# Optimization experiments

Hardware: AMD Instinct MI355X
Metric: run time of the kernel (lower is better)

The kernel has to match this reference:

```python
import jax, jax.numpy as jnp
import numpy as np

D = 1024      # in_dim
HS = 64       # head_size
H = 16        # num_heads
B, S = 2, 2048


def setup_inputs() -> dict:
    key = jax.random.key(0)
    k1, k2, k3, k4, k5, k6 = jax.random.split(key, 6)
    scale = 1.0 / np.sqrt(D)
    x = jax.random.normal(k1, (B, S, D), dtype=jnp.float32)
    # Stacked per-head projection weights (torch Linear weight is [out,in];
    # random init so layout only needs to be consistent). query weight exists
    # in the torch module but is never used (source bug), so it is omitted.
    Wk = jax.random.normal(k2, (H, D, HS), dtype=jnp.float32) * scale
    Wv = jax.random.normal(k3, (H, D, HS), dtype=jnp.float32) * scale
    Wproj = jax.random.normal(k4, (H * HS, D), dtype=jnp.float32) * (1.0 / np.sqrt(H * HS))
    bproj = jax.random.normal(k5, (D,), dtype=jnp.float32) * 0.01
    return {"x": x, "Wk": Wk, "Wv": Wv, "Wproj": Wproj, "bproj": bproj}


def reference(x, Wk, Wv, Wproj, bproj):
    # Faithful to source: k = key(x); q = value(x); v = value(x)  (q == v, no softmax)
    k = jnp.einsum("bsd,hde->bhse", x, Wk)   # [B,H,S,HS]
    v = jnp.einsum("bsd,hde->bhse", x, Wv)   # [B,H,S,HS]
    q = v
    inv_sqrt = jnp.asarray(HS, x.dtype) ** -0.5
    wei = jnp.einsum("bhse,bhte->bhst", q, k) * inv_sqrt  # [B,H,S,S], unnormalized
    out = jnp.einsum("bhst,bhte->bhse", wei, v)            # [B,H,S,HS]
    # concat heads: [B,S,H*HS]
    out = jnp.transpose(out, (0, 2, 1, 3)).reshape(x.shape[0], x.shape[1], H * HS)
    return out @ Wproj + bproj  # [B,S,D]
```

## Files before the change

### kernel.cpp

```cpp
#include <hip/hip_runtime.h>

#define B_ 2
#define S_ 2048
#define D_ 1024
#define H_ 16
#define HS_ 64
#define HD_ 1024
#define SPLIT 8
#define BS_ (B_*S_)

typedef __attribute__((ext_vector_type(8))) short short8_t;
typedef __attribute__((ext_vector_type(4))) float float4_t;

__device__ inline unsigned short f32_to_bf16(float f) {
  unsigned int u = __float_as_uint(f);
  u += 0x7FFF + ((u >> 16) & 1);
  return (unsigned short)(u >> 16);
}
__device__ inline float bf16_to_f32(unsigned short s) {
  return __uint_as_float(((unsigned int)s) << 16);
}

__device__ inline void async_copy16(const void* g, void* lds) {
  __builtin_amdgcn_global_load_lds(
      (const __attribute__((address_space(1))) void*)g,
      (__attribute__((address_space(3))) void*)lds, 16, 0, 0);
}

__global__ __launch_bounds__(256) void convert_x_kernel(
    const float* __restrict__ x, unsigned short* __restrict__ xb) {
  int idx = blockIdx.x * 256 + threadIdx.x;
  float4 v = ((const float4*)x)[idx];
  ushort4 o;
  o.x = f32_to_bf16(v.x); o.y = f32_to_bf16(v.y);
  o.z = f32_to_bf16(v.z); o.w = f32_to_bf16(v.w);
  ((ushort4*)xb)[idx] = o;
}

__global__ __launch_bounds__(256) void wkvt_kernel(
    const float* __restrict__ Wk, const float* __restrict__ Wv,
    unsigned short* __restrict__ Wkvt) {
  const int h = blockIdx.x >> 4;
  const int d0 = (blockIdx.x & 15) * 64;
  const int tid = threadIdx.x;
  __shared__ float lds[64][65];
#pragma unroll
  for (int i = 0; i < 16; ++i) {
    int idx = tid + i * 256; int dd = idx >> 6, e = idx & 63;
    lds[e][dd] = Wk[((size_t)h * D_ + d0 + dd) * HS_ + e];
  }
  __syncthreads();
#pragma unroll
  for (int i = 0; i < 16; ++i) {
    int idx = tid + i * 256; int e = idx >> 6, dd = idx & 63;
    Wkvt[((size_t)h * 128 + e) * D_ + d0 + dd] = f32_to_bf16(lds[e][dd]);
  }
  __syncthreads();
#pragma unroll
  for (int i = 0; i < 16; ++i) {
    int idx = tid + i * 256; int dd = idx >> 6, e = idx & 63;
    lds[e][dd] = Wv[((size_t)h * D_ + d0 + dd) * HS_ + e];
  }
  __syncthreads();
#pragma unroll
  for (int i = 0; i < 16; ++i) {
    int idx = tid + i * 256; int e = idx >> 6, dd = idx & 63;
    Wkvt[((size_t)h * 128 + 64 + e) * D_ + d0 + dd] = f32_to_bf16(lds[e][dd]);
  }
}

__global__ __launch_bounds__(256) void kv_mfma_kernel(
    const unsigned short* __restrict__ xb,
    const unsigned short* __restrict__ Wkvt,
    unsigned short* __restrict__ Kb,
    unsigned short* __restrict__ Vb) {
  const int blk = blockIdx.x;
  const int stile = blk & 31;
  const int h = blk >> 5;
  const int s0 = stile * 128;
  const int tid = threadIdx.x;
  const int lane = tid & 63;
  const int wid = tid >> 6;
  const int wm = wid & 1, wn = wid >> 1;
  const int quad = lane >> 4, l16 = lane & 15;
  const int arow = lane >> 2;
  const int acol = (lane & 3) * 8;

  __shared__ __align__(16) unsigned short As[128 * 32];
  __shared__ __align__(16) unsigned short Bs[128 * 32];

  float4_t acc[4][4];
  const float4_t fz = {0.f, 0.f, 0.f, 0.f};
#pragma unroll
  for (int i = 0; i < 4; ++i)
#pragma unroll
    for (int j = 0; j < 4; ++j) acc[i][j] = fz;

  for (int k0 = 0; k0 < D_; k0 += 32) {
#pragma unroll
    for (int i = 0; i < 2; ++i) {
      int r = wid * 32 + i * 16 + arow;
      async_copy16(xb + (size_t)(s0 + r) * D_ + k0 + acol,
                   As + (wid * 32 + i * 16) * 32);
      async_copy16(Wkvt + ((size_t)h * 128 + r) * D_ + k0 + acol,
                   Bs + (wid * 32 + i * 16) * 32);
    }
    __syncthreads();
    short8_t a[4], b[4];
#pragma unroll
    for (int mi = 0; mi < 4; ++mi)
      a[mi] = *(const short8_t*)(As + (wm * 64 + mi * 16 + l16) * 32 + quad * 8);
#pragma unroll
    for (int ni = 0; ni < 4; ++ni)
      b[ni] = *(const short8_t*)(Bs + (wn * 64 + ni * 16 + l16) * 32 + quad * 8);
#pragma unroll
    for (int mi = 0; mi < 4; ++mi)
#pragma unroll
      for (int ni = 0; ni < 4; ++ni)
        acc[mi][ni] = __builtin_amdgcn_mfma_f32_16x16x32_bf16(
            a[mi], b[ni], acc[mi][ni], 0, 0, 0);
    __syncthreads();
  }
  unsigned short* dst = (wn == 0) ? Kb : Vb;
#pragma unroll
  for (int mi = 0; mi < 4; ++mi)
#pragma unroll
    for (int ni = 0; ni < 4; ++ni) {
      int c = h * 64 + ni * 16 + l16;
      int rowb = s0 + wm * 64 + mi * 16 + quad * 4;
#pragma unroll
      for (int r = 0; r < 4; ++r)
        dst[(size_t)(rowb + r) * HD_ + c] = f32_to_bf16(acc[mi][ni][r]);
    }
}

__global__ __launch_bounds__(256) void m_partial_kernel(
    const unsigned short* __restrict__ Kb, const unsigned short* __restrict__ Vb,
    float* __restrict__ Mpart) {
  const int blk = blockIdx.x;
  const int h = blk & 15;
  const int b = (blk >> 4) & 1;
  const int split = blk >> 5;
  const int tid = threadIdx.x;
  const int tx = tid & 15, ty = tid >> 4;
  __shared__ float Ks[64][68];
  __shared__ float Vs[64][68];
  float acc[4][4] = {};
  const int sBase = split * (S_ / SPLIT);
  for (int sc = 0; sc < S_ / SPLIT; sc += 64) {
#pragma unroll
    for (int i = 0; i < 16; ++i) {
      int idx = tid + i * 256;
      int r = idx >> 6, c = idx & 63;
      size_t g = (size_t)(b * S_ + sBase + sc + r) * HD_ + h * HS_ + c;
      Ks[r][c] = bf16_to_f32(Kb[g]);
      Vs[r][c] = bf16_to_f32(Vb[g]);
    }
    __syncthreads();
#pragma unroll
    for (int ss = 0; ss < 64; ++ss) {
      const float4 a4 = *(const float4*)&Ks[ss][ty * 4];
      const float4 b4 = *(const float4*)&Vs[ss][tx * 4];
      const float a[4] = {a4.x, a4.y, a4.z, a4.w};
      const float bb[4] = {b4.x, b4.y, b4.z, b4.w};
#pragma unroll
      for (int i = 0; i < 4; ++i)
#pragma unroll
        for (int j = 0; j < 4; ++j) acc[i][j] += a[i] * bb[j];
    }
    __syncthreads();
  }
  float* dst = Mpart + ((size_t)(split * B_ + b) * H_ + h) * HS_ * HS_;
#pragma unroll
  for (int i = 0; i < 4; ++i) {
    float4 o = {acc[i][0], acc[i][1], acc[i][2], acc[i][3]};
    *(float4*)&dst[(ty * 4 + i) * HS_ + tx * 4] = o;
  }
}

__global__ __launch_bounds__(256) void m_reduce_kernel(
    const float* __restrict__ Mpart, float* __restrict__ M) {
  const int bh = blockIdx.x;
  const int tid = threadIdx.x;
  for (int idx = tid; idx < HS_ * HS_; idx += 256) {
    float s = 0.f;
#pragma unroll
    for (int p = 0; p < SPLIT; ++p)
      s += Mpart[((size_t)(p * B_ * H_) + bh) * (HS_ * HS_) + idx];
    M[(size_t)bh * (HS_ * HS_) + idx] = s * 0.125f;
  }
}

__global__ __launch_bounds__(256) void p_kernel(
    const float* __restrict__ M, const float* __restrict__ Wproj,
    unsigned short* __restrict__ Pt) {
  const int blk = blockIdx.x;
  const int dtile = blk & 15;
  const int h = (blk >> 4) & 15;
  const int b = blk >> 8;
  const int d0 = dtile * 64;
  const int tid = threadIdx.x;
  const int tx = tid & 15, ty = tid >> 4;
  __shared__ float Ms[64][68];
  __shared__ float Ws[64][68];
  const size_t mbase = ((size_t)(b * H_ + h)) * HS_ * HS_;
#pragma unroll
  for (int i = 0; i < 16; ++i) {
    int idx = tid + i * 256;
    int f = idx >> 6, e = idx & 63;
    Ms[e][f] = M[mbase + idx];
    Ws[f][e] = Wproj[(size_t)(h * HS_ + f) * D_ + d0 + e];
  }
  __syncthreads();
  float acc[4][4] = {};
#pragma unroll
  for (int kk = 0; kk < 64; ++kk) {
    const float4 a4 = *(const float4*)&Ms[kk][ty * 4];
    const float4 b4 = *(const float4*)&Ws[kk][tx * 4];
    const float a[4] = {a4.x, a4.y, a4.z, a4.w};
    const float bb[4] = {b4.x, b4.y, b4.z, b4.w};
#pragma unroll
    for (int i = 0; i < 4; ++i)
#pragma unroll
      for (int j = 0; j < 4; ++j) acc[i][j] += a[i] * bb[j];
  }
  __syncthreads();
#pragma unroll
  for (int i = 0; i < 4; ++i)
#pragma unroll
    for (int j = 0; j < 4; ++j)
      Ms[tx * 4 + j][ty * 4 + i] = acc[i][j];
  __syncthreads();
  {
    int c = tid >> 2, ch = tid & 3;
    unsigned short* dst = Pt + ((size_t)(b * D_ + d0 + c)) * HD_ + h * 64 + ch * 16;
#pragma unroll
    for (int e = 0; e < 16; ++e) dst[e] = f32_to_bf16(Ms[c][ch * 16 + e]);
  }
}

__global__ __launch_bounds__(256) void out_mfma_kernel(
    const unsigned short* __restrict__ Vb,
    const unsigned short* __restrict__ Pt,
    const float* __restrict__ bproj,
    float* __restrict__ out) {
  const int blk = blockIdx.x;
  const int ntile = blk & 7;
  const int stile = blk >> 3;
  const int s0 = stile * 128;
  const int n0 = ntile * 128;
  const int b = s0 >> 11;
  const int tid = threadIdx.x;
  const int lane = tid & 63;
  const int wid = tid >> 6;
  const int wm = wid & 1, wn = wid >> 1;
  const int quad = lane >> 4, l16 = lane & 15;
  const int arow = lane >> 2;
  const int acol = (lane & 3) * 8;

  __shared__ __align__(16) unsigned short As[128 * 32];
  __shared__ __align__(16) unsigned short Bs[128 * 32];

  float4_t acc[4][4];
  const float4_t fz = {0.f, 0.f, 0.f, 0.f};
#pragma unroll
  for (int i = 0; i < 4; ++i)
#pragma unroll
    for (int j = 0; j < 4; ++j) acc[i][j] = fz;

  const unsigned short* Bpanel = Pt + (size_t)b * D_ * HD_;
  for (int k0 = 0; k0 < HD_; k0 += 32) {
#pragma unroll
    for (int i = 0; i < 2; ++i) {
      int r = wid * 32 + i * 16 + arow;
      async_copy16(Vb + (size_t)(s0 + r) * HD_ + k0 + acol,
                   As + (wid * 32 + i * 16) * 32);
      async_copy16(Bpanel + (size_t)(n0 + r) * HD_ + k0 + acol,
                   Bs + (wid * 32 + i * 16) * 32);
    }
    __syncthreads();
    short8_t a[4], bfr[4];
#pragma unroll
    for (int mi = 0; mi < 4; ++mi)
      a[mi] = *(const short8_t*)(As + (wm * 64 + mi * 16 + l16) * 32 + quad * 8);
#pragma unroll
    for (int ni = 0; ni < 4; ++ni)
      bfr[ni] = *(const short8_t*)(Bs + (wn * 64 + ni * 16 + l16) * 32 + quad * 8);
#pragma unroll
    for (int mi = 0; mi < 4; ++mi)
#pragma unroll
      for (int ni = 0; ni < 4; ++ni)
        acc[mi][ni] = __builtin_amdgcn_mfma_f32_16x16x32_bf16(
            a[mi], bfr[ni], acc[mi][ni], 0, 0, 0);
    __syncthreads();
  }
#pragma unroll
  for (int ni = 0; ni < 4; ++ni) {
    int col = n0 + wn * 64 + ni * 16 + l16;
    float bias = bproj[col];
#pragma unroll
    for (int mi = 0; mi < 4; ++mi) {
      int rowb = s0 + wm * 64 + mi * 16 + quad * 4;
#pragma unroll
      for (int r = 0; r < 4; ++r)
        out[(size_t)(rowb + r) * D_ + col] = acc[mi][ni][r] + bias;
    }
  }
}

extern "C" void kernel_launch(void* const* d_in, const int* in_sizes, int n_in,
                              void* d_out, int out_size, void* d_ws, size_t ws_size,
                              hipStream_t stream) {
  const float* x = (const float*)d_in[0];
  const float* Wk = (const float*)d_in[1];
  const float* Wv = (const float*)d_in[2];
  const float* Wproj = (const float*)d_in[3];
  const float* bproj = (const float*)d_in[4];
  float* out = (float*)d_out;

  char* ws = (char*)d_ws;
  unsigned short* xb = (unsigned short*)ws;
  unsigned short* Wkvt = xb + (size_t)BS_ * D_;
  unsigned short* Kb = Wkvt + (size_t)H_ * 128 * D_;
  unsigned short* Vb = Kb + (size_t)BS_ * HD_;
  float* Mpart = (float*)(Vb + (size_t)BS_ * HD_);
  float* M = Mpart + (size_t)SPLIT * B_ * H_ * HS_ * HS_;
  unsigned short* Pt = (unsigned short*)(M + (size_t)B_ * H_ * HS_ * HS_);

  convert_x_kernel<<<dim3(BS_ * D_ / 1024), dim3(256), 0, stream>>>(x, xb);
  wkvt_kernel<<<dim3(H_ * (D_ / 64)), dim3(256), 0, stream>>>(Wk, Wv, Wkvt);
  kv_mfma_kernel<<<dim3((BS_ / 128) * H_), dim3(256), 0, stream>>>(xb, Wkvt, Kb, Vb);
  m_partial_kernel<<<dim3(SPLIT * B_ * H_), dim3(256), 0, stream>>>(Kb, Vb, Mpart);
  m_reduce_kernel<<<dim3(B_ * H_), dim3(256), 0, stream>>>(Mpart, M);
  p_kernel<<<dim3(B_ * H_ * (D_ / 64)), dim3(256), 0, stream>>>(M, Wproj, Pt);
  out_mfma_kernel<<<dim3((BS_ / 128) * (D_ / 128)), dim3(256), 0, stream>>>(Vb, Pt, bproj, out);
}
```

Before: 157.4 us.

## Merge prep kernels, deepen GEMM K-tiles, shrink output tile, widen split-K reduction

Merges the x-conversion and weight-transpose kernels into one launch, saving a launch. Doubles the K tile to 64 in both MFMA GEMMs, halving the number of barrier pairs per loop. The output GEMM moves to 128x64 tiles, doubling the block count for better CU occupancy at the cost of more operand reloads. SPLIT goes from 8 to 16 and the reduction uses float4 loads across more blocks; the wider LDS rows may add bank conflicts.

Measured after the change: 150.9 us. 1.04x faster.

```diff
diff --git a/kernel.cpp b/kernel.cpp
--- a/kernel.cpp
+++ b/kernel.cpp
@@ -6,8 +6,9 @@
 #define H_ 16
 #define HS_ 64
 #define HD_ 1024
-#define SPLIT 8
+#define SPLIT 16
 #define BS_ (B_*S_)
+#define BK_ 64
 
 typedef __attribute__((ext_vector_type(8))) short short8_t;
 typedef __attribute__((ext_vector_type(4))) float float4_t;
@@ -27,23 +28,25 @@
       (__attribute__((address_space(3))) void*)lds, 16, 0, 0);
 }
 
-__global__ __launch_bounds__(256) void convert_x_kernel(
-    const float* __restrict__ x, unsigned short* __restrict__ xb) {
-  int idx = blockIdx.x * 256 + threadIdx.x;
-  float4 v = ((const float4*)x)[idx];
-  ushort4 o;
-  o.x = f32_to_bf16(v.x); o.y = f32_to_bf16(v.y);
-  o.z = f32_to_bf16(v.z); o.w = f32_to_bf16(v.w);
-  ((ushort4*)xb)[idx] = o;
-}
-
-__global__ __launch_bounds__(256) void wkvt_kernel(
-    const float* __restrict__ Wk, const float* __restrict__ Wv,
+__global__ __launch_bounds__(256) void prep_kernel(
+    const float* __restrict__ x, const float* __restrict__ Wk,
+    const float* __restrict__ Wv, unsigned short* __restrict__ xb,
     unsigned short* __restrict__ Wkvt) {
-  const int h = blockIdx.x >> 4;
-  const int d0 = (blockIdx.x & 15) * 64;
+  const int blk = blockIdx.x;
   const int tid = threadIdx.x;
   __shared__ float lds[64][65];
+  if (blk < 4096) {
+    int idx = blk * 256 + tid;
+    float4 v = ((const float4*)x)[idx];
+    ushort4 o;
+    o.x = f32_to_bf16(v.x); o.y = f32_to_bf16(v.y);
+    o.z = f32_to_bf16(v.z); o.w = f32_to_bf16(v.w);
+    ((ushort4*)xb)[idx] = o;
+    return;
+  }
+  const int wblk = blk - 4096;
+  const int h = wblk >> 4;
+  const int d0 = (wblk & 15) * 64;
 #pragma unroll
   for (int i = 0; i < 16; ++i) {
     int idx = tid + i * 256; int dd = idx >> 6, e = idx & 63;
@@ -83,11 +86,11 @@
   const int wid = tid >> 6;
   const int wm = wid & 1, wn = wid >> 1;
   const int quad = lane >> 4, l16 = lane & 15;
-  const int arow = lane >> 2;
-  const int acol = (lane & 3) * 8;
-
-  __shared__ __align__(16) unsigned short As[128 * 32];
-  __shared__ __align__(16) unsigned short Bs[128 * 32];
+  const int srow = lane >> 3;
+  const int scol = (lane & 7) * 8;
+
+  __shared__ __align__(16) unsigned short As[128 * BK_];
+  __shared__ __align__(16) unsigned short Bs[128 * BK_];
 
   float4_t acc[4][4];
   const float4_t fz = {0.f, 0.f, 0.f, 0.f};
@@ -96,29 +99,36 @@
 #pragma unroll
     for (int j = 0; j < 4; ++j) acc[i][j] = fz;
 
-  for (int k0 = 0; k0 < D_; k0 += 32) {
-#pragma unroll
-    for (int i = 0; i < 2; ++i) {
-      int r = wid * 32 + i * 16 + arow;
-      async_copy16(xb + (size_t)(s0 + r) * D_ + k0 + acol,
-                   As + (wid * 32 + i * 16) * 32);
-      async_copy16(Wkvt + ((size_t)h * 128 + r) * D_ + k0 + acol,
-                   Bs + (wid * 32 + i * 16) * 32);
-    }
-    __syncthreads();
-    short8_t a[4], b[4];
+  for (int k0 = 0; k0 < D_; k0 += BK_) {
+#pragma unroll
+    for (int i = 0; i < 4; ++i) {
+      int g = wid * 4 + i;
+      int r = g * 8 + srow;
+      async_copy16(xb + (size_t)(s0 + r) * D_ + k0 + scol, As + g * 8 * BK_);
+      async_copy16(Wkvt + ((size_t)h * 128 + r) * D_ + k0 + scol, Bs + g * 8 * BK_);
+    }
+    __syncthreads();
+    short8_t a[4][2], b[4][2];
 #pragma unroll
     for (int mi = 0; mi < 4; ++mi)
-      a[mi] = *(const short8_t*)(As + (wm * 64 + mi * 16 + l16) * 32 + quad * 8);
+#pragma unroll
+      for (int ks = 0; ks < 2; ++ks)
+        a[mi][ks] = *(const short8_t*)(As + (wm * 64 + mi * 16 + l16) * BK_ +
+                                       (ks * 4 + quad) * 8);
 #pragma unroll
     for (int ni = 0; ni < 4; ++ni)
-      b[ni] = *(const short8_t*)(Bs + (wn * 64 + ni * 16 + l16) * 32 + quad * 8);
-#pragma unroll
-    for (int mi = 0; mi < 4; ++mi)
-#pragma unroll
-      for (int ni = 0; ni < 4; ++ni)
-        acc[mi][ni] = __builtin_amdgcn_mfma_f32_16x16x32_bf16(
-            a[mi], b[ni], acc[mi][ni], 0, 0, 0);
+#pragma unroll
+      for (int ks = 0; ks < 2; ++ks)
+        b[ni][ks] = *(const short8_t*)(Bs + (wn * 64 + ni * 16 + l16) * BK_ +
+                                       (ks * 4 + quad) * 8);
+#pragma unroll
+    for (int ks = 0; ks < 2; ++ks)
+#pragma unroll
+      for (int mi = 0; mi < 4; ++mi)
+#pragma unroll
+        for (int ni = 0; ni < 4; ++ni)
+          acc[mi][ni] = __builtin_amdgcn_mfma_f32_16x16x32_bf16(
+              a[mi][ks], b[ni][ks], acc[mi][ni], 0, 0, 0);
     __syncthreads();
   }
   unsigned short* dst = (wn == 0) ? Kb : Vb;
@@ -180,15 +190,18 @@
 
 __global__ __launch_bounds__(256) void m_reduce_kernel(
     const float* __restrict__ Mpart, float* __restrict__ M) {
-  const int bh = blockIdx.x;
-  const int tid = threadIdx.x;
-  for (int idx = tid; idx < HS_ * HS_; idx += 256) {
-    float s = 0.f;
-#pragma unroll
-    for (int p = 0; p < SPLIT; ++p)
-      s += Mpart[((size_t)(p * B_ * H_) + bh) * (HS_ * HS_) + idx];
-    M[(size_t)bh * (HS_ * HS_) + idx] = s * 0.125f;
-  }
+  const int gid = blockIdx.x * 256 + threadIdx.x;
+  const int e0 = gid * 4;
+  const int bh = e0 >> 12;
+  const int idx = e0 & 4095;
+  float4 s = {0.f, 0.f, 0.f, 0.f};
+#pragma unroll
+  for (int p = 0; p < SPLIT; ++p) {
+    const float4 v = *(const float4*)&Mpart[((size_t)(p * B_ * H_) + bh) * 4096 + idx];
+    s.x += v.x; s.y += v.y; s.z += v.z; s.w += v.w;
+  }
+  s.x *= 0.125f; s.y *= 0.125f; s.z *= 0.125f; s.w *= 0.125f;
+  *(float4*)&M[(size_t)bh * 4096 + idx] = s;
 }
 
 __global__ __launch_bounds__(256) void p_kernel(
@@ -245,58 +258,70 @@
     const float* __restrict__ bproj,
     float* __restrict__ out) {
   const int blk = blockIdx.x;
-  const int ntile = blk & 7;
-  const int stile = blk >> 3;
+  const int ntile = blk & 15;
+  const int stile = blk >> 4;
   const int s0 = stile * 128;
-  const int n0 = ntile * 128;
+  const int n0 = ntile * 64;
   const int b = s0 >> 11;
   const int tid = threadIdx.x;
   const int lane = tid & 63;
   const int wid = tid >> 6;
   const int wm = wid & 1, wn = wid >> 1;
   const int quad = lane >> 4, l16 = lane & 15;
-  const int arow = lane >> 2;
-  const int acol = (lane & 3) * 8;
-
-  __shared__ __align__(16) unsigned short As[128 * 32];
-  __shared__ __align__(16) unsigned short Bs[128 * 32];
-
-  float4_t acc[4][4];
+  const int srow = lane >> 3;
+  const int scol = (lane & 7) * 8;
+
+  __shared__ __align__(16) unsigned short As[128 * BK_];
+  __shared__ __align__(16) unsigned short Bs[64 * BK_];
+
+  float4_t acc[4][2];
   const float4_t fz = {0.f, 0.f, 0.f, 0.f};
 #pragma unroll
   for (int i = 0; i < 4; ++i)
 #pragma unroll
-    for (int j = 0; j < 4; ++j) acc[i][j] = fz;
+    for (int j = 0; j < 2; ++j) acc[i][j] = fz;
 
   const unsigned short* Bpanel = Pt + (size_t)b * D_ * HD_;
-  for (int k0 = 0; k0 < HD_; k0 += 32) {
+  for (int k0 = 0; k0 < HD_; k0 += BK_) {
+#pragma unroll
+    for (int i = 0; i < 4; ++i) {
+      int g = wid * 4 + i;
+      int r = g * 8 + srow;
+      async_copy16(Vb + (size_t)(s0 + r) * HD_ + k0 + scol, As + g * 8 * BK_);
+    }
 #pragma unroll
     for (int i = 0; i < 2; ++i) {
-      int r = wid * 32 + i * 16 + arow;
-      async_copy16(Vb + (size_t)(s0 + r) * HD_ + k0 + acol,
-                   As + (wid * 32 + i * 16) * 32);
-      async_copy16(Bpanel + (size_t)(n0 + r) * HD_ + k0 + acol,
-                   Bs + (wid * 32 + i * 16) * 32);
-    }
-    __syncthreads();
-    short8_t a[4], bfr[4];
+      int g = wid * 2 + i;
+      int r = g * 8 + srow;
+      async_copy16(Bpanel + (size_t)(n0 + r) * HD_ + k0 + scol, Bs + g * 8 * BK_);
+    }
+    __syncthreads();
+    short8_t a[4][2], bfr[2][2];
 #pragma unroll
     for (int mi = 0; mi < 4; ++mi)
-      a[mi] = *(const short8_t*)(As + (wm * 64 + mi * 16 + l16) * 32 + quad * 8);
-#pragma unroll
-    for (int ni = 0; ni < 4; ++ni)
-      bfr[ni] = *(const short8_t*)(Bs + (wn * 64 + ni * 16 + l16) * 32 + quad * 8);
-#pragma unroll
-    for (int mi = 0; mi < 4; ++mi)
-#pragma unroll
-      for (int ni = 0; ni < 4; ++ni)
-        acc[mi][ni] = __builtin_amdgcn_mfma_f32_16x16x32_bf16(
-            a[mi], bfr[ni], acc[mi][ni], 0, 0, 0);
-    __syncthreads();
-  }
-#pragma unroll
-  for (int ni = 0; ni < 4; ++ni) {
-    int col = n0 + wn * 64 + ni * 16 + l16;
+#pragma unroll
+      for (int ks = 0; ks < 2; ++ks)
+        a[mi][ks] = *(const short8_t*)(As + (wm * 64 + mi * 16 + l16) * BK_ +
+                                       (ks * 4 + quad) * 8);
+#pragma unroll
+    for (int ni = 0; ni < 2; ++ni)
+#pragma unroll
+      for (int ks = 0; ks < 2; ++ks)
+        bfr[ni][ks] = *(const short8_t*)(Bs + (wn * 32 + ni * 16 + l16) * BK_ +
+                                         (ks * 4 + quad) * 8);
+#pragma unroll
+    for (int ks = 0; ks < 2; ++ks)
+#pragma unroll
+      for (int mi = 0; mi < 4; ++mi)
+#pragma unroll
+        for (int ni = 0; ni < 2; ++ni)
+          acc[mi][ni] = __builtin_amdgcn_mfma_f32_16x16x32_bf16(
+              a[mi][ks], bfr[ni][ks], acc[mi][ni], 0, 0, 0);
+    __syncthreads();
+  }
+#pragma unroll
+  for (int ni = 0; ni < 2; ++ni) {
+    int col = n0 + wn * 32 + ni * 16 + l16;
     float bias = bproj[col];
 #pragma unroll
     for (int mi = 0; mi < 4; ++mi) {
@@ -327,11 +352,10 @@
   float* M = Mpart + (size_t)SPLIT * B_ * H_ * HS_ * HS_;
   unsigned short* Pt = (unsigned short*)(M + (size_t)B_ * H_ * HS_ * HS_);
 
-  convert_x_kernel<<<dim3(BS_ * D_ / 1024), dim3(256), 0, stream>>>(x, xb);
-  wkvt_kernel<<<dim3(H_ * (D_ / 64)), dim3(256), 0, stream>>>(Wk, Wv, Wkvt);
+  prep_kernel<<<dim3(4096 + H_ * (D_ / 64)), dim3(256), 0, stream>>>(x, Wk, Wv, xb, Wkvt);
   kv_mfma_kernel<<<dim3((BS_ / 128) * H_), dim3(256), 0, stream>>>(xb, Wkvt, Kb, Vb);
   m_partial_kernel<<<dim3(SPLIT * B_ * H_), dim3(256), 0, stream>>>(Kb, Vb, Mpart);
-  m_reduce_kernel<<<dim3(B_ * H_), dim3(256), 0, stream>>>(Mpart, M);
+  m_reduce_kernel<<<dim3(128), dim3(256), 0, stream>>>(Mpart, M);
   p_kernel<<<dim3(B_ * H_ * (D_ / 64)), dim3(256), 0, stream>>>(M, Wproj, Pt);
-  out_mfma_kernel<<<dim3((BS_ / 128) * (D_ / 128)), dim3(256), 0, stream>>>(Vb, Pt, bproj, out);
-}
+  out_mfma_kernel<<<dim3((BS_ / 128) * (D_ / 64)), dim3(256), 0, stream>>>(Vb, Pt, bproj, out);
+}
```
